# Kernel optimization log

Measured on AMD Instinct MI355X. Metric: run time of the kernel, lower is better.

## Reference

```python
import jax, jax.numpy as jnp
import numpy as np

H, W, D, HEADS = 32, 32, 16, 8
EPS = 1e-5

def _ln(x, g, b):
    m = jnp.mean(x, -1, keepdims=True)
    v = jnp.mean((x - m) ** 2, -1, keepdims=True)
    return (x - m) / jnp.sqrt(v + EPS) * g + b

def _attn(x, w_qkv, w_proj, b_proj):
    # x: (Bb, N, C); torch Linear: y = x @ W.T + b
    Bb, N, C = x.shape
    hd = C // HEADS
    qkv = jnp.einsum('bnc,dc->bnd', x, w_qkv).reshape(Bb, N, 3, HEADS, hd)
    q, k, v = qkv[:, :, 0], qkv[:, :, 1], qkv[:, :, 2]  # (Bb,N,h,hd)
    att = jnp.einsum('bnhd,bmhd->bhnm', q, k) * (hd ** -0.5)
    att = jax.nn.softmax(att, axis=-1)
    o = jnp.einsum('bhnm,bmhd->bnhd', att, v).reshape(Bb, N, C)
    return jnp.einsum('bnc,dc->bnd', o, w_proj) + b_proj

def setup_inputs() -> dict:
    key = jax.random.key(0)
    ks = jax.random.split(key, 8)
    C, HID = 96, 384
    s = 0.02
    return {
        'x': jax.random.normal(ks[0], (1, C, D, H, W), jnp.float32),
        'norm1_g': jnp.ones((C,), jnp.float32),
        'norm1_b': jnp.zeros((C,), jnp.float32),
        'qkv_hw_w': jax.random.normal(ks[1], (3 * C, C), jnp.float32) * s,
        'proj_hw_w': jax.random.normal(ks[2], (C, C), jnp.float32) * s,
        'proj_hw_b': jnp.zeros((C,), jnp.float32),
        'qkv_t_w': jax.random.normal(ks[3], (3 * C, C), jnp.float32) * s,
        'proj_t_w': jax.random.normal(ks[4], (C, C), jnp.float32) * s,
        'proj_t_b': jnp.zeros((C,), jnp.float32),
        'norm2_g': jnp.ones((C,), jnp.float32),
        'norm2_b': jnp.zeros((C,), jnp.float32),
        'fc1_w': jax.random.normal(ks[5], (HID, C), jnp.float32) * s,
        'fc1_b': jnp.zeros((HID,), jnp.float32),
        'fc2_w': jax.random.normal(ks[6], (C, HID), jnp.float32) * s,
        'fc2_b': jnp.zeros((C,), jnp.float32),
    }

def reference(x, norm1_g, norm1_b, qkv_hw_w, proj_hw_w, proj_hw_b,
              qkv_t_w, proj_t_w, proj_t_b, norm2_g, norm2_b,
              fc1_w, fc1_b, fc2_w, fc2_b):
    B, C = x.shape[0], x.shape[1]
    HWn = H * W
    xf = x.reshape(B, C, -1).transpose(0, 2, 1)  # (B, L, C), L = D*H*W (D-major)
    shortcut = xf
    n1 = _ln(xf, norm1_g, norm1_b).reshape(B, D, HWn, C)
    # attention over H*W tokens (batched over B*D)
    a_hw = _attn(n1.reshape(B * D, HWn, C), qkv_hw_w, proj_hw_w, proj_hw_b)
    a_hw = a_hw.reshape(B, -1, C)  # D-major token order
    # attention over D tokens (batched over B*H*W)
    a_t = _attn(n1.transpose(0, 2, 1, 3).reshape(B * HWn, D, C), qkv_t_w, proj_t_w, proj_t_b)
    a_t = a_t.reshape(B, HWn * D, C)  # HW-major order (faithful to original view)
    out_res = shortcut + a_hw + a_t
    h1 = jax.nn.gelu(jnp.einsum('blc,hc->blh', _ln(out_res, norm2_g, norm2_b), fc1_w) + fc1_b,
                     approximate=False)
    mlp_out = jnp.einsum('blh,ch->blc', h1, fc2_w) + fc2_b
    out_ffn = out_res + mlp_out
    out = out_ffn.reshape(B, H, W, D, C).transpose(0, 4, 3, 1, 2)  # (B,C,D,H,W)
    return out
```

## Files before the change

kernel.cpp:

```cpp
#include <hip/hip_runtime.h>
#include <math.h>

#define L_TOK 16384
#define C_DIM 96
#define N_HEADS 8
#define HD 12
#define D_DIM 16
#define HW_N 1024
#define HID_DIM 384
#define SCALE 0.2886751345948129f
#define LOG2E 1.4426950408889634f

typedef _Float16 h4 __attribute__((ext_vector_type(4)));
typedef __fp16 fp16x2 __attribute__((ext_vector_type(2)));
typedef float v4f __attribute__((ext_vector_type(4)));

static __device__ __forceinline__ float fast_exp2(float x) {
#if __has_builtin(__builtin_amdgcn_exp2f)
    return __builtin_amdgcn_exp2f(x);
#else
    float r;
    asm("v_exp_f32 %0, %1" : "=v"(r) : "v"(x));
    return r;
#endif
}

static __device__ __forceinline__ h4 pack4(float a, float b, float c, float d) {
    fp16x2 lo = __builtin_amdgcn_cvt_pkrtz(a, b);
    fp16x2 hi = __builtin_amdgcn_cvt_pkrtz(c, d);
    union { fp16x2 p[2]; h4 v; } u;
    u.p[0] = lo; u.p[1] = hi;
    return u.v;
}

__global__ __launch_bounds__(256) void wconv_kernel(
    const float* __restrict__ qkv_hw_w, const float* __restrict__ qkv_t_w,
    const float* __restrict__ proj_hw_w, const float* __restrict__ proj_t_w,
    const float* __restrict__ proj_hw_b, const float* __restrict__ proj_t_b,
    const float* __restrict__ fc1_w, const float* __restrict__ fc2_w,
    _Float16* __restrict__ wq, _Float16* __restrict__ wp,
    _Float16* __restrict__ wf1, _Float16* __restrict__ wf2,
    float* __restrict__ bp) {
    int idx = blockIdx.x * 256 + threadIdx.x;
    if (idx < 55296) {
        int n = idx / 96;
        float v = (n < 288) ? qkv_hw_w[idx] : qkv_t_w[idx - 27648];
        bool isq = (n < 96) || (n >= 288 && n < 384);
        wq[idx] = (_Float16)(isq ? v * (SCALE * LOG2E) : v);
    } else if (idx < 55296 + 18432) {
        int i = idx - 55296;
        int n = i / 192, k = i % 192;
        float v = (k < 96) ? proj_hw_w[n * 96 + k] : proj_t_w[n * 96 + k - 96];
        wp[i] = (_Float16)v;
    } else if (idx < 73728 + 36864) {
        int i = idx - 73728;
        wf1[i] = (_Float16)fc1_w[i];
    } else if (idx < 110592 + 36864) {
        int i = idx - 110592;
        wf2[i] = (_Float16)fc2_w[i];
    } else if (idx < 147456 + 96) {
        int i = idx - 147456;
        bp[i] = proj_hw_b[i] + proj_t_b[i];
    }
}

__global__ __launch_bounds__(256) void ln1_kernel(
    const float* __restrict__ x, const float* __restrict__ g,
    const float* __restrict__ b, _Float16* __restrict__ n1h) {
    int l = blockIdx.x * 256 + threadIdx.x;
    float v[C_DIM];
    float s = 0.f;
#pragma unroll
    for (int c = 0; c < C_DIM; c++) {
        v[c] = x[(size_t)c * L_TOK + l];
        s += v[c];
    }
    float mean = s * (1.f / C_DIM);
    float var = 0.f;
#pragma unroll
    for (int c = 0; c < C_DIM; c++) {
        float dd = v[c] - mean;
        var += dd * dd;
    }
    float r = rsqrtf(var * (1.f / C_DIM) + 1e-5f);
    _Float16* op = n1h + (size_t)l * C_DIM;
#pragma unroll
    for (int c = 0; c < C_DIM; c += 4) {
        h4 o;
        o[0] = (_Float16)((v[c + 0] - mean) * r * g[c + 0] + b[c + 0]);
        o[1] = (_Float16)((v[c + 1] - mean) * r * g[c + 1] + b[c + 1]);
        o[2] = (_Float16)((v[c + 2] - mean) * r * g[c + 2] + b[c + 2]);
        o[3] = (_Float16)((v[c + 3] - mean) * r * g[c + 3] + b[c + 3]);
        *(h4*)(op + c) = o;
    }
}

__global__ __launch_bounds__(256) void ln2_kernel(
    const float* __restrict__ in, const float* __restrict__ g,
    const float* __restrict__ b, _Float16* __restrict__ out) {
    int l = blockIdx.x * 256 + threadIdx.x;
    const float* ip = in + (size_t)l * C_DIM;
    float v[C_DIM];
    float s = 0.f;
#pragma unroll
    for (int c = 0; c < C_DIM; c += 4) {
        float4 t = *(const float4*)(ip + c);
        v[c] = t.x; v[c + 1] = t.y; v[c + 2] = t.z; v[c + 3] = t.w;
        s += t.x + t.y + t.z + t.w;
    }
    float mean = s * (1.f / C_DIM);
    float var = 0.f;
#pragma unroll
    for (int c = 0; c < C_DIM; c++) {
        float dd = v[c] - mean;
        var += dd * dd;
    }
    float r = rsqrtf(var * (1.f / C_DIM) + 1e-5f);
    _Float16* op = out + (size_t)l * C_DIM;
#pragma unroll
    for (int c = 0; c < C_DIM; c += 4) {
        h4 o;
        o[0] = (_Float16)((v[c + 0] - mean) * r * g[c + 0] + b[c + 0]);
        o[1] = (_Float16)((v[c + 1] - mean) * r * g[c + 1] + b[c + 1]);
        o[2] = (_Float16)((v[c + 2] - mean) * r * g[c + 2] + b[c + 2]);
        o[3] = (_Float16)((v[c + 3] - mean) * r * g[c + 3] + b[c + 3]);
        *(h4*)(op + c) = o;
    }
}

#define GBM 64
#define GBN 48
#define GBK 96
#define LSTRIDE 104

__global__ __launch_bounds__(256) void gemm_qkv(
    const _Float16* __restrict__ A, const _Float16* __restrict__ W,
    _Float16* __restrict__ Qp, _Float16* __restrict__ Kp,
    _Float16* __restrict__ VTp, _Float16* __restrict__ Tp) {
    __shared__ _Float16 As[GBM][LSTRIDE];
    __shared__ _Float16 Ws[GBN][LSTRIDE];
    const int t = threadIdx.x;
    const int m0 = blockIdx.x * GBM;
    const int n0 = blockIdx.y * GBN;
    const int lane = t & 63, w = t >> 6, g = lane >> 4, r = lane & 15;

    v4f acc[3];
#pragma unroll
    for (int nt = 0; nt < 3; nt++) {
        acc[nt][0] = 0.f; acc[nt][1] = 0.f; acc[nt][2] = 0.f; acc[nt][3] = 0.f;
    }
#pragma unroll
    for (int i = 0; i < 3; i++) {
        int idx = t + i * 256;
        int row = idx / 12, c = idx % 12;
        *(float4*)&As[row][c * 8] =
            *(const float4*)&A[(size_t)(m0 + row) * 96 + c * 8];
    }
#pragma unroll
    for (int i = 0; i < 3; i++) {
        int idx = t + i * 256;
        if (idx < 576) {
            int row = idx / 12, c = idx % 12;
            *(float4*)&Ws[row][c * 8] =
                *(const float4*)&W[(size_t)(n0 + row) * 96 + c * 8];
        }
    }
    __syncthreads();
#pragma unroll
    for (int ks = 0; ks < 6; ks++) {
        h4 af = *(const h4*)&As[w * 16 + r][ks * 16 + 4 * g];
#pragma unroll
        for (int nt = 0; nt < 3; nt++) {
            h4 wf = *(const h4*)&Ws[nt * 16 + r][ks * 16 + 4 * g];
            acc[nt] = __builtin_amdgcn_mfma_f32_16x16x16f16(wf, af, acc[nt], 0, 0, 0);
        }
    }

    const int m = m0 + w * 16 + r;
    const int d = m >> 10, hw = m & 1023;
    const int by = blockIdx.y;
#pragma unroll
    for (int nt = 0; nt < 3; nt++) {
        const int nb = n0 + nt * 16 + 4 * g;
        h4 ov;
        ov[0] = (_Float16)acc[nt][0]; ov[1] = (_Float16)acc[nt][1];
        ov[2] = (_Float16)acc[nt][2]; ov[3] = (_Float16)acc[nt][3];
        if (by < 2) {
            int n = nb;
            int h = (unsigned)n / 12u, dd = n - h * 12;
            *(h4*)&Qp[((size_t)(d * 8 + h) * 1024 + hw) * 12 + dd] = ov;
        } else if (by < 4) {
            int n = nb - 96;
            int h = (unsigned)n / 12u, dd = n - h * 12;
            *(h4*)&Kp[((size_t)(d * 8 + h) * 1024 + hw) * 12 + dd] = ov;
        } else if (by < 6) {
            int n = nb - 192;
            int h = (unsigned)n / 12u, dd = n - h * 12;
#pragma unroll
            for (int j = 0; j < 4; j++) {
                VTp[((size_t)(d * 8 + h) * 12 + dd + j) * 1024 + hw] = ov[j];
            }
        } else {
            *(h4*)&Tp[(size_t)(hw * 16 + d) * 288 + (nb - 288)] = ov;
        }
    }
}

template <int MODE>
__global__ __launch_bounds__(256) void gemm_mfma(
    const _Float16* __restrict__ A, const _Float16* __restrict__ W,
    const float* __restrict__ bias, void* __restrict__ outp,
    const float* __restrict__ res, int K) {
    __shared__ _Float16 As[GBM][LSTRIDE];
    __shared__ _Float16 Ws[GBN][LSTRIDE];
    const int t = threadIdx.x;
    const int m0 = blockIdx.x * GBM;
    const int n0 = blockIdx.y * GBN;
    const int lane = t & 63, w = t >> 6, g = lane >> 4, r = lane & 15;

    v4f acc[3];
#pragma unroll
    for (int nt = 0; nt < 3; nt++) {
        acc[nt][0] = 0.f; acc[nt][1] = 0.f; acc[nt][2] = 0.f; acc[nt][3] = 0.f;
    }

    for (int k0 = 0; k0 < K; k0 += GBK) {
        __syncthreads();
#pragma unroll
        for (int i = 0; i < 3; i++) {
            int idx = t + i * 256;
            int row = idx / 12, c = idx % 12;
            *(float4*)&As[row][c * 8] =
                *(const float4*)&A[(size_t)(m0 + row) * K + k0 + c * 8];
        }
#pragma unroll
        for (int i = 0; i < 3; i++) {
            int idx = t + i * 256;
            if (idx < 576) {
                int row = idx / 12, c = idx % 12;
                *(float4*)&Ws[row][c * 8] =
                    *(const float4*)&W[(size_t)(n0 + row) * K + k0 + c * 8];
            }
        }
        __syncthreads();
#pragma unroll
        for (int ks = 0; ks < 6; ks++) {
            h4 af = *(const h4*)&As[w * 16 + r][ks * 16 + 4 * g];
#pragma unroll
            for (int nt = 0; nt < 3; nt++) {
                h4 wf = *(const h4*)&Ws[nt * 16 + r][ks * 16 + 4 * g];
                acc[nt] =
                    __builtin_amdgcn_mfma_f32_16x16x16f16(wf, af, acc[nt], 0, 0, 0);
            }
        }
    }

    const int m = m0 + w * 16 + r;
#pragma unroll
    for (int nt = 0; nt < 3; nt++) {
        const int nb = n0 + nt * 16 + 4 * g;
        if (MODE == 1) {
            float4 bv = *(const float4*)&bias[nb];
            float* o = (float*)outp;
            float4 ov;
            ov.x = acc[nt][0] + bv.x + res[(size_t)(nb + 0) * L_TOK + m];
            ov.y = acc[nt][1] + bv.y + res[(size_t)(nb + 1) * L_TOK + m];
            ov.z = acc[nt][2] + bv.z + res[(size_t)(nb + 2) * L_TOK + m];
            ov.w = acc[nt][3] + bv.w + res[(size_t)(nb + 3) * L_TOK + m];
            *(float4*)&o[(size_t)m * 96 + nb] = ov;
        } else if (MODE == 2) {
            float4 bv = *(const float4*)&bias[nb];
            _Float16* o = (_Float16*)outp;
            float vv[4];
            vv[0] = acc[nt][0] + bv.x; vv[1] = acc[nt][1] + bv.y;
            vv[2] = acc[nt][2] + bv.z; vv[3] = acc[nt][3] + bv.w;
            h4 ov;
#pragma unroll
            for (int j = 0; j < 4; j++) {
                float u = vv[j];
                ov[j] = (_Float16)(0.5f * u * (1.f + erff(u * 0.7071067811865476f)));
            }
            *(h4*)&o[(size_t)m * 384 + nb] = ov;
        } else {
            float4 bv = *(const float4*)&bias[nb];
            float4 rv = *(const float4*)&res[(size_t)m * 96 + nb];
            float* o = (float*)outp;
            int dd = m & 15, ww2 = (m >> 4) & 31, hh = m >> 9;
            size_t base = (size_t)dd * 1024 + hh * 32 + ww2;
            o[(size_t)(nb + 0) * L_TOK + base] = acc[nt][0] + bv.x + rv.x;
            o[(size_t)(nb + 1) * L_TOK + base] = acc[nt][1] + bv.y + rv.y;
            o[(size_t)(nb + 2) * L_TOK + base] = acc[nt][2] + bv.z + rv.z;
            o[(size_t)(nb + 3) * L_TOK + base] = acc[nt][3] + bv.w + rv.w;
        }
    }
}

__global__ __launch_bounds__(256) void attn_hw_kernel(
    const _Float16* __restrict__ Qp, const _Float16* __restrict__ Kp,
    const _Float16* __restrict__ VTp, _Float16* __restrict__ o_cat) {
    __shared__ _Float16 K_lds[1024 * 12];
    __shared__ _Float16 VT_lds[13 * 1032];
    const int t = threadIdx.x;
    const int qb = blockIdx.x, h = blockIdx.y, d = blockIdx.z;
    const size_t tokbase = (size_t)d * HW_N;
    const int hoff = h * HD;
    const size_t slice = (size_t)(d * 8 + h);

    {
        const float4* Kg = (const float4*)(Kp + slice * 12288);
        float4* K4 = (float4*)K_lds;
#pragma unroll
        for (int i = 0; i < 6; i++) K4[t + i * 256] = Kg[t + i * 256];
        const float4* Vg = (const float4*)(VTp + slice * 12288);
#pragma unroll
        for (int i = 0; i < 6; i++) {
            int off = t + i * 256;
            int row = off >> 7, col = (off & 127) * 8;
            *(float4*)&VT_lds[row * 1032 + col] = Vg[off];
        }
        unsigned* zp = (unsigned*)&VT_lds[12 * 1032];
        zp[t] = 0x3C003C00u; zp[t + 256] = 0x3C003C00u;
        if (t < 4) zp[t + 512] = 0x3C003C00u;
    }

    const int lane = t & 63, w = t >> 6, g = lane >> 4, r = lane & 15;
    const int q0w = qb * 256 + w * 64;

    h4 zf; zf[0] = zf[1] = zf[2] = zf[3] = (_Float16)0.f;
    h4 qf[4];
    {
        const _Float16* Qbase = Qp + (slice * 1024 + q0w + r) * 12 + 4 * g;
#pragma unroll
        for (int qt = 0; qt < 4; qt++) {
            qf[qt] = (g < 3) ? *(const h4*)(Qbase + qt * 16 * 12) : zf;
        }
    }

    v4f acc[4];
#pragma unroll
    for (int qt = 0; qt < 4; qt++) {
        acc[qt][0] = acc[qt][1] = acc[qt][2] = acc[qt][3] = 0.f;
    }

    const int koff = r * 12 + 4 * g;
    const int rowc = (r < 12) ? r : 12;
    const int voff = rowc * 1032 + 4 * g;

    __syncthreads();

    v4f zero; zero[0] = zero[1] = zero[2] = zero[3] = 0.f;
#pragma unroll 4
    for (int kt = 0; kt < HW_N / 16; kt++) {
        h4 kf = (g < 3) ? *(const h4*)&K_lds[kt * 192 + koff] : zf;
        h4 vf = *(const h4*)&VT_lds[voff + kt * 16];
#pragma unroll
        for (int qt = 0; qt < 4; qt++) {
            v4f s = __builtin_amdgcn_mfma_f32_16x16x16f16(kf, qf[qt], zero, 0, 0, 0);
            h4 pf = pack4(fast_exp2(s[0]), fast_exp2(s[1]),
                          fast_exp2(s[2]), fast_exp2(s[3]));
            acc[qt] = __builtin_amdgcn_mfma_f32_16x16x16f16(vf, pf, acc[qt], 0, 0, 0);
        }
    }

#pragma unroll
    for (int qt = 0; qt < 4; qt++) {
        float denom = __shfl(acc[qt][0], 48 + r, 64);
        float rs = 1.f / denom;
        if (g < 3) {
            _Float16* op =
                o_cat + (tokbase + q0w + qt * 16 + r) * 192 + hoff + 4 * g;
            h4 o;
            o[0] = (_Float16)(acc[qt][0] * rs);
            o[1] = (_Float16)(acc[qt][1] * rs);
            o[2] = (_Float16)(acc[qt][2] * rs);
            o[3] = (_Float16)(acc[qt][3] * rs);
            *(h4*)op = o;
        }
    }
}

__global__ __launch_bounds__(256) void attn_t_kernel(
    const _Float16* __restrict__ Tp, _Float16* __restrict__ o_cat) {
    int gid = blockIdx.x * 256 + threadIdx.x;
    int hw = gid >> 7;
    int h = (gid >> 4) & 7;
    int q = gid & 15;
    const int hoff = h * HD;
    const _Float16* base = Tp + (size_t)(hw * 16) * 288;

    float qr[HD];
    {
        const _Float16* p = base + q * 288 + hoff;
        h4 a = *(const h4*)p, b = *(const h4*)(p + 4), c = *(const h4*)(p + 8);
#pragma unroll
        for (int e = 0; e < 4; e++) {
            qr[e] = (float)a[e]; qr[4 + e] = (float)b[e]; qr[8 + e] = (float)c[e];
        }
    }
    float s[D_DIM];
    float mx = -1e30f;
#pragma unroll
    for (int j = 0; j < D_DIM; j++) {
        const _Float16* kp = base + j * 288 + 96 + hoff;
        h4 a = *(const h4*)kp, b = *(const h4*)(kp + 4), c = *(const h4*)(kp + 8);
        float dot = 0.f;
#pragma unroll
        for (int e = 0; e < 4; e++) {
            dot += qr[e] * (float)a[e] + qr[4 + e] * (float)b[e] +
                   qr[8 + e] * (float)c[e];
        }
        s[j] = dot;
        mx = fmaxf(mx, dot);
    }
    float sum = 0.f;
#pragma unroll
    for (int j = 0; j < D_DIM; j++) {
        s[j] = fast_exp2(s[j] - mx);
        sum += s[j];
    }
    float rs = 1.f / sum;
    float o[HD];
#pragma unroll
    for (int e = 0; e < HD; e++) o[e] = 0.f;
#pragma unroll
    for (int j = 0; j < D_DIM; j++) {
        const _Float16* vp = base + j * 288 + 192 + hoff;
        h4 a = *(const h4*)vp, b = *(const h4*)(vp + 4), c = *(const h4*)(vp + 8);
        float p = s[j];
#pragma unroll
        for (int e = 0; e < 4; e++) {
            o[e] += p * (float)a[e];
            o[4 + e] += p * (float)b[e];
            o[8 + e] += p * (float)c[e];
        }
    }
    _Float16* op = o_cat + ((size_t)hw * D_DIM + q) * 192 + 96 + hoff;
#pragma unroll
    for (int e = 0; e < HD; e += 4) {
        h4 a;
        a[0] = (_Float16)(o[e] * rs); a[1] = (_Float16)(o[e + 1] * rs);
        a[2] = (_Float16)(o[e + 2] * rs); a[3] = (_Float16)(o[e + 3] * rs);
        *(h4*)(op + e) = a;
    }
}

extern "C" void kernel_launch(void* const* d_in, const int* in_sizes, int n_in,
                              void* d_out, int out_size, void* d_ws,
                              size_t ws_size, hipStream_t stream) {
    const float* x         = (const float*)d_in[0];
    const float* norm1_g   = (const float*)d_in[1];
    const float* norm1_b   = (const float*)d_in[2];
    const float* qkv_hw_w  = (const float*)d_in[3];
    const float* proj_hw_w = (const float*)d_in[4];
    const float* proj_hw_b = (const float*)d_in[5];
    const float* qkv_t_w   = (const float*)d_in[6];
    const float* proj_t_w  = (const float*)d_in[7];
    const float* proj_t_b  = (const float*)d_in[8];
    const float* norm2_g   = (const float*)d_in[9];
    const float* norm2_b   = (const float*)d_in[10];
    const float* fc1_w     = (const float*)d_in[11];
    const float* fc1_b     = (const float*)d_in[12];
    const float* fc2_w     = (const float*)d_in[13];
    const float* fc2_b     = (const float*)d_in[14];
    float* out = (float*)d_out;

    char* ws = (char*)d_ws;
    _Float16* n1h    = (_Float16*)ws;
    _Float16* o_cat  = n1h + (size_t)L_TOK * C_DIM;
    float*    out_res= (float*)(o_cat + (size_t)L_TOK * 192);
    _Float16* packs  = (_Float16*)(out_res + (size_t)L_TOK * C_DIM);
    _Float16* Qp     = packs;
    _Float16* Kp     = Qp + 1572864;
    _Float16* VTp    = Kp + 1572864;
    _Float16* Tp     = VTp + 1572864;
    _Float16* h1     = packs;
    _Float16* wq     = Tp + (size_t)L_TOK * 288;
    _Float16* wp     = wq + 55296;
    _Float16* wf1    = wp + 18432;
    _Float16* wf2    = wf1 + 36864;
    float*    bp     = (float*)(wf2 + 36864);

    wconv_kernel<<<577, 256, 0, stream>>>(qkv_hw_w, qkv_t_w, proj_hw_w,
                                          proj_t_w, proj_hw_b, proj_t_b,
                                          fc1_w, fc2_w, wq, wp, wf1, wf2, bp);
    ln1_kernel<<<L_TOK / 256, 256, 0, stream>>>(x, norm1_g, norm1_b, n1h);
    gemm_qkv<<<dim3(L_TOK / GBM, 576 / GBN), 256, 0, stream>>>(
        n1h, wq, Qp, Kp, VTp, Tp);
    attn_hw_kernel<<<dim3(4, N_HEADS, D_DIM), 256, 0, stream>>>(
        Qp, Kp, VTp, o_cat);
    attn_t_kernel<<<(HW_N * N_HEADS * D_DIM) / 256, 256, 0, stream>>>(Tp, o_cat);
    gemm_mfma<1><<<dim3(L_TOK / GBM, C_DIM / GBN), 256, 0, stream>>>(
        o_cat, wp, bp, out_res, x, 192);
    ln2_kernel<<<L_TOK / 256, 256, 0, stream>>>(out_res, norm2_g, norm2_b, n1h);
    gemm_mfma<2><<<dim3(L_TOK / GBM, HID_DIM / GBN), 256, 0, stream>>>(
        n1h, wf1, fc1_b, h1, nullptr, C_DIM);
    gemm_mfma<3><<<dim3(L_TOK / GBM, C_DIM / GBN), 256, 0, stream>>>(
        h1, wf2, fc2_b, out, out_res, HID_DIM);
}
```

Before: 105.5 us.

## Fuse LN1 into weight prep, LN2 into proj GEMM, retile attention and fc2 store

Merges the LayerNorm-1 kernel into the weight-conversion kernel and the LayerNorm-2 kernel into the projection GEMM, which now computes the full 96-wide row per block so row statistics come from a wave shuffle. This removes two launches and one round trip of out_res. The attention kernel halves queries per wave and doubles the grid for more parallelism. The fc2 GEMM stages its output through shared memory so the channel-major output is written as coalesced float4 stores, with a block-index swizzle. The fused proj kernel uses more registers and shared memory and launches fewer blocks.

```diff
diff --git a/kernel.cpp b/kernel.cpp
--- a/kernel.cpp
+++ b/kernel.cpp
@@ -33,7 +33,9 @@
     return u.v;
 }
 
-__global__ __launch_bounds__(256) void wconv_kernel(
+__global__ __launch_bounds__(256) void prep_kernel(
+    const float* __restrict__ x, const float* __restrict__ g1,
+    const float* __restrict__ b1, _Float16* __restrict__ n1h,
     const float* __restrict__ qkv_hw_w, const float* __restrict__ qkv_t_w,
     const float* __restrict__ proj_hw_w, const float* __restrict__ proj_t_w,
     const float* __restrict__ proj_hw_b, const float* __restrict__ proj_t_b,
@@ -41,7 +43,36 @@
     _Float16* __restrict__ wq, _Float16* __restrict__ wp,
     _Float16* __restrict__ wf1, _Float16* __restrict__ wf2,
     float* __restrict__ bp) {
-    int idx = blockIdx.x * 256 + threadIdx.x;
+    if (blockIdx.x < 64) {
+        int l = blockIdx.x * 256 + threadIdx.x;
+        float v[C_DIM];
+        float s = 0.f;
+#pragma unroll
+        for (int c = 0; c < C_DIM; c++) {
+            v[c] = x[(size_t)c * L_TOK + l];
+            s += v[c];
+        }
+        float mean = s * (1.f / C_DIM);
+        float var = 0.f;
+#pragma unroll
+        for (int c = 0; c < C_DIM; c++) {
+            float dd = v[c] - mean;
+            var += dd * dd;
+        }
+        float r = rsqrtf(var * (1.f / C_DIM) + 1e-5f);
+        _Float16* op = n1h + (size_t)l * C_DIM;
+#pragma unroll
+        for (int c = 0; c < C_DIM; c += 4) {
+            h4 o;
+            o[0] = (_Float16)((v[c + 0] - mean) * r * g1[c + 0] + b1[c + 0]);
+            o[1] = (_Float16)((v[c + 1] - mean) * r * g1[c + 1] + b1[c + 1]);
+            o[2] = (_Float16)((v[c + 2] - mean) * r * g1[c + 2] + b1[c + 2]);
+            o[3] = (_Float16)((v[c + 3] - mean) * r * g1[c + 3] + b1[c + 3]);
+            *(h4*)(op + c) = o;
+        }
+        return;
+    }
+    int idx = (blockIdx.x - 64) * 256 + threadIdx.x;
     if (idx < 55296) {
         int n = idx / 96;
         float v = (n < 288) ? qkv_hw_w[idx] : qkv_t_w[idx - 27648];
@@ -64,70 +95,6 @@
     }
 }
 
-__global__ __launch_bounds__(256) void ln1_kernel(
-    const float* __restrict__ x, const float* __restrict__ g,
-    const float* __restrict__ b, _Float16* __restrict__ n1h) {
-    int l = blockIdx.x * 256 + threadIdx.x;
-    float v[C_DIM];
-    float s = 0.f;
-#pragma unroll
-    for (int c = 0; c < C_DIM; c++) {
-        v[c] = x[(size_t)c * L_TOK + l];
-        s += v[c];
-    }
-    float mean = s * (1.f / C_DIM);
-    float var = 0.f;
-#pragma unroll
-    for (int c = 0; c < C_DIM; c++) {
-        float dd = v[c] - mean;
-        var += dd * dd;
-    }
-    float r = rsqrtf(var * (1.f / C_DIM) + 1e-5f);
-    _Float16* op = n1h + (size_t)l * C_DIM;
-#pragma unroll
-    for (int c = 0; c < C_DIM; c += 4) {
-        h4 o;
-        o[0] = (_Float16)((v[c + 0] - mean) * r * g[c + 0] + b[c + 0]);
-        o[1] = (_Float16)((v[c + 1] - mean) * r * g[c + 1] + b[c + 1]);
-        o[2] = (_Float16)((v[c + 2] - mean) * r * g[c + 2] + b[c + 2]);
-        o[3] = (_Float16)((v[c + 3] - mean) * r * g[c + 3] + b[c + 3]);
-        *(h4*)(op + c) = o;
-    }
-}
-
-__global__ __launch_bounds__(256) void ln2_kernel(
-    const float* __restrict__ in, const float* __restrict__ g,
-    const float* __restrict__ b, _Float16* __restrict__ out) {
-    int l = blockIdx.x * 256 + threadIdx.x;
-    const float* ip = in + (size_t)l * C_DIM;
-    float v[C_DIM];
-    float s = 0.f;
-#pragma unroll
-    for (int c = 0; c < C_DIM; c += 4) {
-        float4 t = *(const float4*)(ip + c);
-        v[c] = t.x; v[c + 1] = t.y; v[c + 2] = t.z; v[c + 3] = t.w;
-        s += t.x + t.y + t.z + t.w;
-    }
-    float mean = s * (1.f / C_DIM);
-    float var = 0.f;
-#pragma unroll
-    for (int c = 0; c < C_DIM; c++) {
-        float dd = v[c] - mean;
-        var += dd * dd;
-    }
-    float r = rsqrtf(var * (1.f / C_DIM) + 1e-5f);
-    _Float16* op = out + (size_t)l * C_DIM;
-#pragma unroll
-    for (int c = 0; c < C_DIM; c += 4) {
-        h4 o;
-        o[0] = (_Float16)((v[c + 0] - mean) * r * g[c + 0] + b[c + 0]);
-        o[1] = (_Float16)((v[c + 1] - mean) * r * g[c + 1] + b[c + 1]);
-        o[2] = (_Float16)((v[c + 2] - mean) * r * g[c + 2] + b[c + 2]);
-        o[3] = (_Float16)((v[c + 3] - mean) * r * g[c + 3] + b[c + 3]);
-        *(h4*)(op + c) = o;
-    }
-}
-
 #define GBM 64
 #define GBN 48
 #define GBK 96
@@ -206,11 +173,100 @@
     }
 }
 
-template <int MODE>
-__global__ __launch_bounds__(256) void gemm_mfma(
+__global__ __launch_bounds__(256) void gemm_proj_ln2(
     const _Float16* __restrict__ A, const _Float16* __restrict__ W,
-    const float* __restrict__ bias, void* __restrict__ outp,
-    const float* __restrict__ res, int K) {
+    const float* __restrict__ bp, const float* __restrict__ x,
+    const float* __restrict__ g2, const float* __restrict__ b2,
+    float* __restrict__ out_res, _Float16* __restrict__ n2h) {
+    __shared__ _Float16 As[64][LSTRIDE];
+    __shared__ _Float16 Ws[96][LSTRIDE];
+    const int t = threadIdx.x;
+    const int m0 = blockIdx.x * 64;
+    const int lane = t & 63, w = t >> 6, g = lane >> 4, r = lane & 15;
+
+    v4f acc[6];
+#pragma unroll
+    for (int nt = 0; nt < 6; nt++) {
+        acc[nt][0] = 0.f; acc[nt][1] = 0.f; acc[nt][2] = 0.f; acc[nt][3] = 0.f;
+    }
+
+    for (int k0 = 0; k0 < 192; k0 += 96) {
+        __syncthreads();
+#pragma unroll
+        for (int i = 0; i < 3; i++) {
+            int idx = t + i * 256;
+            int row = idx / 12, c = idx % 12;
+            *(float4*)&As[row][c * 8] =
+                *(const float4*)&A[(size_t)(m0 + row) * 192 + k0 + c * 8];
+        }
+#pragma unroll
+        for (int i = 0; i < 5; i++) {
+            int idx = t + i * 256;
+            if (idx < 1152) {
+                int row = idx / 12, c = idx % 12;
+                *(float4*)&Ws[row][c * 8] =
+                    *(const float4*)&W[(size_t)row * 192 + k0 + c * 8];
+            }
+        }
+        __syncthreads();
+#pragma unroll
+        for (int ks = 0; ks < 6; ks++) {
+            h4 af = *(const h4*)&As[w * 16 + r][ks * 16 + 4 * g];
+#pragma unroll
+            for (int nt = 0; nt < 6; nt++) {
+                h4 wf = *(const h4*)&Ws[nt * 16 + r][ks * 16 + 4 * g];
+                acc[nt] =
+                    __builtin_amdgcn_mfma_f32_16x16x16f16(wf, af, acc[nt], 0, 0, 0);
+            }
+        }
+    }
+
+    const int m = m0 + w * 16 + r;
+    float v[24];
+    float sum = 0.f;
+#pragma unroll
+    for (int nt = 0; nt < 6; nt++) {
+        const int nb = nt * 16 + 4 * g;
+        float4 bv = *(const float4*)&bp[nb];
+        float a0 = acc[nt][0] + bv.x + x[(size_t)(nb + 0) * L_TOK + m];
+        float a1 = acc[nt][1] + bv.y + x[(size_t)(nb + 1) * L_TOK + m];
+        float a2 = acc[nt][2] + bv.z + x[(size_t)(nb + 2) * L_TOK + m];
+        float a3 = acc[nt][3] + bv.w + x[(size_t)(nb + 3) * L_TOK + m];
+        v[nt * 4 + 0] = a0; v[nt * 4 + 1] = a1;
+        v[nt * 4 + 2] = a2; v[nt * 4 + 3] = a3;
+        sum += (a0 + a1) + (a2 + a3);
+        float4 ov; ov.x = a0; ov.y = a1; ov.z = a2; ov.w = a3;
+        *(float4*)&out_res[(size_t)m * 96 + nb] = ov;
+    }
+    sum += __shfl_xor(sum, 16, 64);
+    sum += __shfl_xor(sum, 32, 64);
+    float mean = sum * (1.f / 96.f);
+    float ss = 0.f;
+#pragma unroll
+    for (int i = 0; i < 24; i++) {
+        float dd = v[i] - mean;
+        ss += dd * dd;
+    }
+    ss += __shfl_xor(ss, 16, 64);
+    ss += __shfl_xor(ss, 32, 64);
+    float rstd = rsqrtf(ss * (1.f / 96.f) + 1e-5f);
+#pragma unroll
+    for (int nt = 0; nt < 6; nt++) {
+        const int nb = nt * 16 + 4 * g;
+        float4 gg = *(const float4*)&g2[nb];
+        float4 bb = *(const float4*)&b2[nb];
+        h4 o;
+        o[0] = (_Float16)((v[nt * 4 + 0] - mean) * rstd * gg.x + bb.x);
+        o[1] = (_Float16)((v[nt * 4 + 1] - mean) * rstd * gg.y + bb.y);
+        o[2] = (_Float16)((v[nt * 4 + 2] - mean) * rstd * gg.z + bb.z);
+        o[3] = (_Float16)((v[nt * 4 + 3] - mean) * rstd * gg.w + bb.w);
+        *(h4*)&n2h[(size_t)m * 96 + nb] = o;
+    }
+}
+
+__global__ __launch_bounds__(256) void gemm_fc1(
+    const _Float16* __restrict__ A, const _Float16* __restrict__ W,
+    const float* __restrict__ bias, _Float16* __restrict__ h1) {
     __shared__ _Float16 As[GBM][LSTRIDE];
     __shared__ _Float16 Ws[GBN][LSTRIDE];
     const int t = threadIdx.x;
@@ -223,15 +279,79 @@
     for (int nt = 0; nt < 3; nt++) {
         acc[nt][0] = 0.f; acc[nt][1] = 0.f; acc[nt][2] = 0.f; acc[nt][3] = 0.f;
     }
-
-    for (int k0 = 0; k0 < K; k0 += GBK) {
+#pragma unroll
+    for (int i = 0; i < 3; i++) {
+        int idx = t + i * 256;
+        int row = idx / 12, c = idx % 12;
+        *(float4*)&As[row][c * 8] =
+            *(const float4*)&A[(size_t)(m0 + row) * 96 + c * 8];
+    }
+#pragma unroll
+    for (int i = 0; i < 3; i++) {
+        int idx = t + i * 256;
+        if (idx < 576) {
+            int row = idx / 12, c = idx % 12;
+            *(float4*)&Ws[row][c * 8] =
+                *(const float4*)&W[(size_t)(n0 + row) * 96 + c * 8];
+        }
+    }
+    __syncthreads();
+#pragma unroll
+    for (int ks = 0; ks < 6; ks++) {
+        h4 af = *(const h4*)&As[w * 16 + r][ks * 16 + 4 * g];
+#pragma unroll
+        for (int nt = 0; nt < 3; nt++) {
+            h4 wf = *(const h4*)&Ws[nt * 16 + r][ks * 16 + 4 * g];
+            acc[nt] = __builtin_amdgcn_mfma_f32_16x16x16f16(wf, af, acc[nt], 0, 0, 0);
+        }
+    }
+
+    const int m = m0 + w * 16 + r;
+#pragma unroll
+    for (int nt = 0; nt < 3; nt++) {
+        const int nb = n0 + nt * 16 + 4 * g;
+        float4 bv = *(const float4*)&bias[nb];
+        float vv[4];
+        vv[0] = acc[nt][0] + bv.x; vv[1] = acc[nt][1] + bv.y;
+        vv[2] = acc[nt][2] + bv.z; vv[3] = acc[nt][3] + bv.w;
+        h4 ov;
+#pragma unroll
+        for (int j = 0; j < 4; j++) {
+            float u = vv[j];
+            ov[j] = (_Float16)(0.5f * u * (1.f + erff(u * 0.7071067811865476f)));
+        }
+        *(h4*)&h1[(size_t)m * 384 + nb] = ov;
+    }
+}
+
+__global__ __launch_bounds__(256) void gemm_fc2(
+    const _Float16* __restrict__ A, const _Float16* __restrict__ W,
+    const float* __restrict__ bias, float* __restrict__ out,
+    const float* __restrict__ res) {
+    __shared__ _Float16 As[GBM][LSTRIDE];
+    __shared__ _Float16 Ws[GBN][LSTRIDE];
+    __shared__ float sh[GBN][68];
+    const int t = threadIdx.x;
+    const int bx = blockIdx.x;
+    const int bxs = (bx & 7) * 32 + (bx >> 3);
+    const int m0 = bxs * GBM;
+    const int n0 = blockIdx.y * GBN;
+    const int lane = t & 63, w = t >> 6, g = lane >> 4, r = lane & 15;
+
+    v4f acc[3];
+#pragma unroll
+    for (int nt = 0; nt < 3; nt++) {
+        acc[nt][0] = 0.f; acc[nt][1] = 0.f; acc[nt][2] = 0.f; acc[nt][3] = 0.f;
+    }
+
+    for (int k0 = 0; k0 < 384; k0 += GBK) {
         __syncthreads();
 #pragma unroll
         for (int i = 0; i < 3; i++) {
             int idx = t + i * 256;
             int row = idx / 12, c = idx % 12;
             *(float4*)&As[row][c * 8] =
-                *(const float4*)&A[(size_t)(m0 + row) * K + k0 + c * 8];
+                *(const float4*)&A[(size_t)(m0 + row) * 384 + k0 + c * 8];
         }
 #pragma unroll
         for (int i = 0; i < 3; i++) {
@@ -239,7 +359,7 @@
             if (idx < 576) {
                 int row = idx / 12, c = idx % 12;
                 *(float4*)&Ws[row][c * 8] =
-                    *(const float4*)&W[(size_t)(n0 + row) * K + k0 + c * 8];
+                    *(const float4*)&W[(size_t)(n0 + row) * 384 + k0 + c * 8];
             }
         }
         __syncthreads();
@@ -256,42 +376,29 @@
     }
 
     const int m = m0 + w * 16 + r;
+    const int m_local = w * 16 + r;
 #pragma unroll
     for (int nt = 0; nt < 3; nt++) {
         const int nb = n0 + nt * 16 + 4 * g;
-        if (MODE == 1) {
-            float4 bv = *(const float4*)&bias[nb];
-            float* o = (float*)outp;
-            float4 ov;
-            ov.x = acc[nt][0] + bv.x + res[(size_t)(nb + 0) * L_TOK + m];
-            ov.y = acc[nt][1] + bv.y + res[(size_t)(nb + 1) * L_TOK + m];
-            ov.z = acc[nt][2] + bv.z + res[(size_t)(nb + 2) * L_TOK + m];
-            ov.w = acc[nt][3] + bv.w + res[(size_t)(nb + 3) * L_TOK + m];
-            *(float4*)&o[(size_t)m * 96 + nb] = ov;
-        } else if (MODE == 2) {
-            float4 bv = *(const float4*)&bias[nb];
-            _Float16* o = (_Float16*)outp;
-            float vv[4];
-            vv[0] = acc[nt][0] + bv.x; vv[1] = acc[nt][1] + bv.y;
-            vv[2] = acc[nt][2] + bv.z; vv[3] = acc[nt][3] + bv.w;
-            h4 ov;
-#pragma unroll
-            for (int j = 0; j < 4; j++) {
-                float u = vv[j];
-                ov[j] = (_Float16)(0.5f * u * (1.f + erff(u * 0.7071067811865476f)));
-            }
-            *(h4*)&o[(size_t)m * 384 + nb] = ov;
-        } else {
-            float4 bv = *(const float4*)&bias[nb];
-            float4 rv = *(const float4*)&res[(size_t)m * 96 + nb];
-            float* o = (float*)outp;
-            int dd = m & 15, ww2 = (m >> 4) & 31, hh = m >> 9;
-            size_t base = (size_t)dd * 1024 + hh * 32 + ww2;
-            o[(size_t)(nb + 0) * L_TOK + base] = acc[nt][0] + bv.x + rv.x;
-            o[(size_t)(nb + 1) * L_TOK + base] = acc[nt][1] + bv.y + rv.y;
-            o[(size_t)(nb + 2) * L_TOK + base] = acc[nt][2] + bv.z + rv.z;
-            o[(size_t)(nb + 3) * L_TOK + base] = acc[nt][3] + bv.w + rv.w;
-        }
+        float4 bv = *(const float4*)&bias[nb];
+        float4 rv = *(const float4*)&res[(size_t)m * 96 + nb];
+        sh[nt * 16 + 4 * g + 0][m_local] = acc[nt][0] + bv.x + rv.x;
+        sh[nt * 16 + 4 * g + 1][m_local] = acc[nt][1] + bv.y + rv.y;
+        sh[nt * 16 + 4 * g + 2][m_local] = acc[nt][2] + bv.z + rv.z;
+        sh[nt * 16 + 4 * g + 3][m_local] = acc[nt][3] + bv.w + rv.w;
+    }
+    __syncthreads();
+    const int hh = m0 >> 9, ww0 = (m0 >> 4) & 31;
+#pragma unroll
+    for (int i = 0; i < 3; i++) {
+        int task = t + i * 256;
+        int n_local = task >> 4, dd = task & 15;
+        float4 ov;
+        ov.x = sh[n_local][dd];
+        ov.y = sh[n_local][dd + 16];
+        ov.z = sh[n_local][dd + 32];
+        ov.w = sh[n_local][dd + 48];
+        *(float4*)&out[(size_t)(n0 + n_local) * L_TOK + dd * 1024 + hh * 32 + ww0] = ov;
     }
 }
 
@@ -324,21 +431,21 @@
     }
 
     const int lane = t & 63, w = t >> 6, g = lane >> 4, r = lane & 15;
-    const int q0w = qb * 256 + w * 64;
+    const int q0w = qb * 128 + w * 32;
 
     h4 zf; zf[0] = zf[1] = zf[2] = zf[3] = (_Float16)0.f;
-    h4 qf[4];
+    h4 qf[2];
     {
         const _Float16* Qbase = Qp + (slice * 1024 + q0w + r) * 12 + 4 * g;
 #pragma unroll
-        for (int qt = 0; qt < 4; qt++) {
+        for (int qt = 0; qt < 2; qt++) {
             qf[qt] = (g < 3) ? *(const h4*)(Qbase + qt * 16 * 12) : zf;
         }
     }
 
-    v4f acc[4];
-#pragma unroll
-    for (int qt = 0; qt < 4; qt++) {
+    v4f acc[2];
+#pragma unroll
+    for (int qt = 0; qt < 2; qt++) {
         acc[qt][0] = acc[qt][1] = acc[qt][2] = acc[qt][3] = 0.f;
     }
 
@@ -354,7 +461,7 @@
         h4 kf = (g < 3) ? *(const h4*)&K_lds[kt * 192 + koff] : zf;
         h4 vf = *(const h4*)&VT_lds[voff + kt * 16];
 #pragma unroll
-        for (int qt = 0; qt < 4; qt++) {
+        for (int qt = 0; qt < 2; qt++) {
             v4f s = __builtin_amdgcn_mfma_f32_16x16x16f16(kf, qf[qt], zero, 0, 0, 0);
             h4 pf = pack4(fast_exp2(s[0]), fast_exp2(s[1]),
                           fast_exp2(s[2]), fast_exp2(s[3]));
@@ -363,7 +470,7 @@
     }
 
 #pragma unroll
-    for (int qt = 0; qt < 4; qt++) {
+    for (int qt = 0; qt < 2; qt++) {
         float denom = __shfl(acc[qt][0], 48 + r, 64);
         float rs = 1.f / denom;
         if (g < 3) {
@@ -480,20 +587,19 @@
     _Float16* wf2    = wf1 + 36864;
     float*    bp     = (float*)(wf2 + 36864);
 
-    wconv_kernel<<<577, 256, 0, stream>>>(qkv_hw_w, qkv_t_w, proj_hw_w,
-                                          proj_t_w, proj_hw_b, proj_t_b,
-                                          fc1_w, fc2_w, wq, wp, wf1, wf2, bp);
-    ln1_kernel<<<L_TOK / 256, 256, 0, stream>>>(x, norm1_g, norm1_b, n1h);
+    prep_kernel<<<641, 256, 0, stream>>>(x, norm1_g, norm1_b, n1h,
+                                         qkv_hw_w, qkv_t_w, proj_hw_w,
+                                         proj_t_w, proj_hw_b, proj_t_b,
+                                         fc1_w, fc2_w, wq, wp, wf1, wf2, bp);
     gemm_qkv<<<dim3(L_TOK / GBM, 576 / GBN), 256, 0, stream>>>(
         n1h, wq, Qp, Kp, VTp, Tp);
-    attn_hw_kernel<<<dim3(4, N_HEADS, D_DIM), 256, 0, stream>>>(
+    attn_hw_kernel<<<dim3(8, N_HEADS, D_DIM), 256, 0, stream>>>(
         Qp, Kp, VTp, o_cat);
     attn_t_kernel<<<(HW_N * N_HEADS * D_DIM) / 256, 256, 0, stream>>>(Tp, o_cat);
-    gemm_mfma<1><<<dim3(L_TOK / GBM, C_DIM / GBN), 256, 0, stream>>>(
-        o_cat, wp, bp, out_res, x, 192);
-    ln2_kernel<<<L_TOK / 256, 256, 0, stream>>>(out_res, norm2_g, norm2_b, n1h);
-    gemm_mfma<2><<<dim3(L_TOK / GBM, HID_DIM / GBN), 256, 0, stream>>>(
-        n1h, wf1, fc1_b, h1, nullptr, C_DIM);
-    gemm_mfma<3><<<dim3(L_TOK / GBM, C_DIM / GBN), 256, 0, stream>>>(
-        h1, wf2, fc2_b, out, out_res, HID_DIM);
-}
+    gemm_proj_ln2<<<L_TOK / 64, 256, 0, stream>>>(
+        o_cat, wp, bp, x, norm2_g, norm2_b, out_res, n1h);
+    gemm_fc1<<<dim3(L_TOK / GBM, HID_DIM / GBN), 256, 0, stream>>>(
+        n1h, wf1, fc1_b, h1);
+    gemm_fc2<<<dim3(L_TOK / GBM, C_DIM / GBN), 256, 0, stream>>>(
+        h1, wf2, fc2_b, out, out_res);
+}
```

Result: faster. 94.20 us (-10.7%).
